# Kernel optimization log

Measured on AMD Instinct MI355X. Metric: run time of the kernel, lower is better.

## Reference

```python
import math
from collections import deque
import jax, jax.numpy as jnp
import numpy as np

PS = 16; DF = 256; DS = 16; DLANG = 896; BETA = 2.0
B_SZ = 2; IMG = 512


def setup_inputs():
    key = jax.random.key(0)
    ks = jax.random.split(key, 16)
    def rn(k, shape, scale=1.0):
        return jax.random.normal(k, shape, jnp.float32) * scale
    # W_delta bias init: inverse-softplus of dt ~ LogUniform(1e-3, 1e-1), as in torch _init_weights
    u = jax.random.uniform(ks[15], (DF,), jnp.float32)
    dt = jnp.exp(u * (math.log(0.1) - math.log(0.001)) + math.log(0.001))
    inv_dt = dt + jnp.log(-jnp.expm1(-dt))
    return {
        "images": rn(ks[0], (B_SZ, 3, IMG, IMG)),
        "lang_g": rn(ks[1], (B_SZ, DLANG)),
        "conv1_w": rn(ks[2], (64, 3, 3, 3), 1.0 / math.sqrt(27)),
        "conv1_b": jnp.zeros((64,), jnp.float32),
        "conv2_w": rn(ks[3], (128, 64, 3, 3), 1.0 / math.sqrt(576)),
        "conv2_b": jnp.zeros((128,), jnp.float32),
        "fc_w": rn(ks[4], (DF, 128), 1.0 / math.sqrt(128)),
        "fc_b": jnp.zeros((DF,), jnp.float32),
        "W_gate": rn(ks[5], (DF, DLANG), 1.0 / math.sqrt(DLANG)),
        "W_g_prime": rn(ks[6], (DF, DLANG), 1.0 / math.sqrt(DLANG)),
        "A_log": jnp.log(jnp.broadcast_to(jnp.arange(1, DS + 1, dtype=jnp.float32), (DF, DS))),
        "D": jnp.ones((DF,), jnp.float32),
        "B_w": rn(ks[7], (DS, DF), 1.0 / math.sqrt(DF)),
        "B_b": jnp.zeros((DS,), jnp.float32),
        "C_w": rn(ks[8], (DS, DF), 1.0 / math.sqrt(DF)),
        "C_b": jnp.zeros((DS,), jnp.float32),
        "Wd_w": rn(ks[9], (DF, DF), 1.0 / math.sqrt(DF)),
        "Wd_b": inv_dt,
        "out_w": rn(ks[10], (DF, DF), 1.0 / math.sqrt(DF)),
        "out_b": jnp.zeros((DF,), jnp.float32),
        "ln_g": jnp.ones((DF,), jnp.float32),
        "ln_b": jnp.zeros((DF,), jnp.float32),
    }


def _gelu(x):
    return jax.nn.gelu(x, approximate=False)  # torch nn.GELU() default = exact erf


def _conv(x, w, b):
    y = jax.lax.conv_general_dilated(x, w, (1, 1), 'SAME', dimension_numbers=('NCHW', 'OIHW', 'NCHW'))
    return y + b[None, :, None, None]


def _patch_feats(images, c1w, c1b, c2w, c2b, fcw, fcb):
    B, C, H, W = images.shape
    nH, nW = H // PS, W // PS
    # non-overlapping patchify (== unfold/unfold in torch)
    p = images.reshape(B, C, nH, PS, nW, PS).transpose(0, 2, 4, 1, 3, 5).reshape(B * nH * nW, C, PS, PS)
    h = _gelu(_conv(p, c1w, c1b))
    h = _gelu(_conv(h, c2w, c2b))
    h = h.mean(axis=(2, 3))  # AdaptiveAvgPool2d((1,1))
    feats = (h @ fcw.T + fcb).reshape(B, nH * nW, DF)
    return feats, nH, nW


def _structure(feats, r_sem, nH, nW):
    # Host-side (numpy) Kruskal MST + BFS ordering, mirroring the torch detach().cpu() path.
    f = np.asarray(feats, np.float32)
    r = np.asarray(r_sem, np.float32)
    B, P, _ = f.shape
    src, dst = [], []
    for i in range(nH):
        for j in range(nW):
            u = i * nW + j
            if j + 1 < nW:
                src.append(u); dst.append(u + 1)
            if i + 1 < nH:
                src.append(u); dst.append(u + nW)
    src = np.array(src); dst = np.array(dst)
    bfs_all, par_all = [], []
    for b in range(B):
        fn = f[b] / np.maximum(np.linalg.norm(f[b], axis=1, keepdims=True), 1e-12)
        cos = (fn[src] * fn[dst]).sum(1)
        w = (1.0 - r[b][src]) * (1.0 - r[b][dst]) * (-cos) + 1e-6
        parent = np.arange(P)
        def find(x):
            while parent[x] != x:
                parent[x] = parent[parent[x]]
                x = parent[x]
            return x
        adj = [[] for _ in range(P)]
        cnt = 0
        for idx in np.argsort(w):
            ru, rv = find(int(src[idx])), find(int(dst[idx]))
            if ru != rv:
                parent[ru] = rv
                adj[src[idx]].append(int(dst[idx]))
                adj[dst[idx]].append(int(src[idx]))
                cnt += 1
                if cnt == P - 1:
                    break
        root = int(r[b].argmax())
        vis = [False] * P; par_of = [-1] * P; bfs = []
        q = deque([root]); vis[root] = True
        while q:
            n = q.popleft()
            bfs.append(n)
            for nb in adj[n]:
                if not vis[nb]:
                    vis[nb] = True
                    par_of[nb] = n
                    q.append(nb)
        o2b = [0] * P
        for bi, oi in enumerate(bfs):
            o2b[oi] = bi
        par_bfs = [-1 if par_of[o] == -1 else o2b[par_of[o]] for o in bfs]
        bfs_all.append(bfs); par_all.append(par_bfs)
    return jnp.array(bfs_all, jnp.int32), jnp.array(par_all, jnp.int32)


def _core(feats, r_sem, g_prime, bfs, par, A_log, D, B_w, B_b, C_w, C_b, Wd_w, Wd_b, out_w, out_b, ln_g, ln_b):
    A = -jnp.exp(A_log)  # (DF, DS)
    def one(f_b, r_b, gp, bfs_b, par_b):
        rs = r_b[bfs_b]                                  # (P,)
        X = f_b[bfs_b] + rs[:, None] * gp[None, :]       # (P, DF)
        delta = jax.nn.softplus(X @ Wd_w.T + Wd_b) * (1.0 + BETA * rs[:, None])
        Bp = X @ B_w.T + B_b                             # (P, DS)
        Cp = X @ C_w.T + C_b                             # (P, DS)
        P = X.shape[0]
        def body(H, inp):
            i, d_i, b_i, c_i, x_i, p_i = inp
            A_bar = jnp.exp(d_i[:, None] * A)            # (DF, DS)
            h_par = H[jnp.maximum(p_i, 0)] * (p_i >= 0)  # zeros at root
            h = A_bar * h_par + (d_i[:, None] * b_i[None, :]) * x_i[:, None]
            H = H.at[i].set(h)
            y = (h * c_i[None, :]).sum(-1) + D * x_i
            return H, y
        H0 = jnp.zeros((P, DF, DS), X.dtype)
        _, Y = jax.lax.scan(body, H0, (jnp.arange(P), delta, Bp, Cp, X, par_b))
        Yr = jnp.zeros_like(Y).at[bfs_b].set(Y)          # scatter back to raster order
        o = Yr @ out_w.T + out_b
        mu = o.mean(-1, keepdims=True)
        v = ((o - mu) ** 2).mean(-1, keepdims=True)
        return ln_g * (o - mu) / jnp.sqrt(v + 1e-5) + ln_b
    return jax.vmap(one)(feats, r_sem, g_prime, bfs, par)


def reference(images, lang_g, conv1_w, conv1_b, conv2_w, conv2_b, fc_w, fc_b, W_gate, W_g_prime, A_log, D, B_w, B_b, C_w, C_b, Wd_w, Wd_b, out_w, out_b, ln_g, ln_b):
    feats, nH, nW = _patch_feats(images, conv1_w, conv1_b, conv2_w, conv2_b, fc_w, fc_b)
    g_proj = lang_g @ W_gate.T
    r_sem = jax.nn.sigmoid(jnp.einsum('bd,bpd->bp', g_proj, feats) / math.sqrt(DF))
    bfs, par = _structure(feats, r_sem, nH, nW)
    g_prime = lang_g @ W_g_prime.T
    return _core(feats, r_sem, g_prime, bfs, par, A_log, D, B_w, B_b, C_w, C_b, Wd_w, Wd_b, out_w, out_b, ln_g, ln_b)
```

## Files before the change

kernel.cpp:

```cpp
#include <hip/hip_runtime.h>
#include <cstddef>
#include <cstdint>

#define NB    2
#define NP    1024
#define DFEAT 256
#define DSTATE 16
#define NEDGE 1984

typedef unsigned short ushortb;

typedef float fx16 __attribute__((ext_vector_type(16)));
typedef short s16x8 __attribute__((ext_vector_type(8)));

__device__ __forceinline__ float bf2f(unsigned short u){
  union { unsigned int i; float f; } c; c.i = ((unsigned int)u) << 16; return c.f;
}
__device__ __forceinline__ unsigned short f2bf(float f){
  union { float f; unsigned int i; } c; c.f = f;
  unsigned int u = c.i;
  unsigned int r = (u + 0x7fffu + ((u >> 16) & 1u)) >> 16;
  return (unsigned short)r;
}
__device__ __forceinline__ float ldin(const void* p, size_t i, int isbf){
  return isbf ? bf2f(((const ushortb*)p)[i]) : ((const float*)p)[i];
}
__device__ __forceinline__ float gelu_f(float x){
  return 0.5f * x * (1.0f + erff(x * 0.70710678118654752f));
}
__device__ __forceinline__ unsigned int f2sort(float f){
  union { float f; unsigned int i; } c; c.f = f;
  return (c.i & 0x80000000u) ? ~c.i : (c.i | 0x80000000u);
}

constexpr size_t AL(size_t x){ return (x + 63) & ~(size_t)63; }
constexpr size_t O_W1    = 0;
constexpr size_t O_B1    = AL(O_W1 + 1728);
constexpr size_t O_W2    = AL(O_B1 + 64);
constexpr size_t O_B2    = AL(O_W2 + 73728);
constexpr size_t O_FCW   = AL(O_B2 + 128);
constexpr size_t O_FCB   = AL(O_FCW + 32768);
constexpr size_t O_WDW   = AL(O_FCB + 256);
constexpr size_t O_WDB   = AL(O_WDW + 65536);
constexpr size_t O_BWO   = AL(O_WDB + 256);
constexpr size_t O_BBO   = AL(O_BWO + 4096);
constexpr size_t O_CWO   = AL(O_BBO + 16);
constexpr size_t O_CBO   = AL(O_CWO + 4096);
constexpr size_t O_OW    = AL(O_CBO + 16);
constexpr size_t O_OB    = AL(O_OW + 65536);
constexpr size_t O_AF    = AL(O_OB + 256);
constexpr size_t O_DD    = AL(O_AF + 4096);
constexpr size_t O_LNG   = AL(O_DD + 256);
constexpr size_t O_LNB   = AL(O_LNG + 256);
constexpr size_t O_FEATS = AL(O_LNB + 256);
constexpr size_t O_GPROJ = AL(O_FEATS + (size_t)NB*NP*DFEAT);
constexpr size_t O_GPRIM = AL(O_GPROJ + NB*DFEAT);
constexpr size_t O_RSEM  = AL(O_GPRIM + NB*DFEAT);
constexpr size_t O_BFS   = AL(O_RSEM + NB*NP);
constexpr size_t O_PAR   = AL(O_BFS + NB*NP);
constexpr size_t O_X     = AL(O_PAR + NB*NP);
constexpr size_t O_DELTA = AL(O_X + (size_t)NB*NP*DFEAT);
constexpr size_t O_BP    = AL(O_DELTA + (size_t)NB*NP*DFEAT);
constexpr size_t O_CP    = AL(O_BP + NB*NP*DSTATE);
constexpr size_t O_YR    = AL(O_CP + NB*NP*DSTATE);
constexpr size_t O_FLAG  = AL(O_YR + (size_t)NB*NP*DFEAT);
constexpr size_t O_LVL   = AL(O_FLAG + 64);

__global__ __launch_bounds__(256) void k_sniff(const void* img, float* ws)
{
  __shared__ int cnt;
  int tid = threadIdx.x;
  if (tid == 0) cnt = 0;
  __syncthreads();
  const ushortb* u = (const ushortb*)img;
  int local = 0;
  for (int k = 0; k < 16; k++){
    unsigned short v = u[tid * 16 + k];
    if (v == 0 || v == 0x8000u){ local++; continue; }
    float f = fabsf(bf2f(v));
    if (f >= 1e-8f && f <= 64.f) local++;
  }
  atomicAdd(&cnt, local);
  __syncthreads();
  if (tid == 0) ((int*)(ws + O_FLAG))[0] = (cnt >= 3900) ? 1 : 0;
}

__global__ __launch_bounds__(256) void k_convert(const void* c1w, const void* c1b, const void* c2w,
                          const void* c2b, const void* fcw, const void* fcb,
                          const void* alog, const void* dvec,
                          const void* bw, const void* bb, const void* cw, const void* cb,
                          const void* wdw, const void* wdb,
                          const void* ow, const void* ob,
                          const void* lng, const void* lnb,
                          const void* lang, const void* wgate, const void* wgp,
                          float* ws)
{
  const int F = ((const int*)(ws + O_FLAG))[0];
  if (blockIdx.x >= 3038){
    int row = (blockIdx.x - 3038) * 4 + (threadIdx.x >> 6);
    int lane = threadIdx.x & 63;
    int mat = row >> 9;
    int b   = (row >> 8) & 1;
    int df  = row & 255;
    const void* W = mat ? wgp : wgate;
    float s = 0.f;
    for (int k = lane; k < 896; k += 64)
      s += ldin(lang, (size_t)b * 896 + k, F) * ldin(W, (size_t)df * 896 + k, F);
    s += __shfl_xor(s, 1);  s += __shfl_xor(s, 2);  s += __shfl_xor(s, 4);
    s += __shfl_xor(s, 8);  s += __shfl_xor(s, 16); s += __shfl_xor(s, 32);
    if (lane == 0) ws[(mat ? O_GPRIM : O_GPROJ) + b * 256 + df] = s;
    return;
  }
  if (blockIdx.x >= 990){
    size_t i2 = (size_t)(blockIdx.x - 990) * 256 + threadIdx.x;
    if (i2 < (size_t)NB * NP * DFEAT) ws[O_YR + i2] = 0.f;
    return;
  }
  int i = blockIdx.x * 256 + threadIdx.x;
  if (i < 1728){ ws[O_W1 + i] = ldin(c1w, i, F); return; } i -= 1728;
  if (i < 64){ ws[O_B1 + i] = ldin(c1b, i, F); return; } i -= 64;
  if (i < 73728){
    int sg = i >> 11;
    int r = i & 2047;
    int nt = r >> 9;
    int r2 = r & 511;
    int ln = r2 >> 3, e = r2 & 7;
    int c  = sg / 18, s = sg - c * 18;
    int tap = s >> 1, ksub = s & 1;
    int oc = nt * 32 + (ln & 31);
    int ic = c * 32 + ksub * 16 + (ln >> 5) * 8 + e;
    float v = ldin(c2w, (size_t)(oc * 64 + ic) * 9 + tap, F);
    ushortb hi = f2bf(v);
    float lo = v - bf2f(hi);
    ushortb* WB = (ushortb*)(ws + O_W2);
    size_t cb = ((size_t)(sg * 4 + nt)) * 2;
    WB[cb * 512 + r2]       = hi;
    WB[(cb + 1) * 512 + r2] = f2bf(lo);
    return;
  } i -= 73728;
  if (i < 128){ ws[O_B2 + i] = ldin(c2b, i, F); return; } i -= 128;
  if (i < 32768){ ws[O_FCW + i] = ldin(fcw, i, F); return; } i -= 32768;
  if (i < 256){ ws[O_FCB + i] = ldin(fcb, i, F); return; } i -= 256;
  if (i < 65536){
    int k = i >> 8, df = i & 255;
    ws[O_WDW + i] = ldin(wdw, (size_t)df * 256 + k, F); return;
  } i -= 65536;
  if (i < 256){ ws[O_WDB + i] = ldin(wdb, i, F); return; } i -= 256;
  if (i < 4096){
    int k = i >> 4, s = i & 15;
    ws[O_BWO + i] = ldin(bw, (size_t)s * 256 + k, F); return;
  } i -= 4096;
  if (i < 16){ ws[O_BBO + i] = ldin(bb, i, F); return; } i -= 16;
  if (i < 4096){
    int k = i >> 4, s = i & 15;
    ws[O_CWO + i] = ldin(cw, (size_t)s * 256 + k, F); return;
  } i -= 4096;
  if (i < 16){ ws[O_CBO + i] = ldin(cb, i, F); return; } i -= 16;
  if (i < 65536){
    int k = i >> 8, df = i & 255;
    ws[O_OW + i] = ldin(ow, (size_t)df * 256 + k, F); return;
  } i -= 65536;
  if (i < 256){ ws[O_OB + i] = ldin(ob, i, F); return; } i -= 256;
  if (i < 4096){ ws[O_AF + i] = -expf(ldin(alog, i, F)); return; } i -= 4096;
  if (i < 256){ ws[O_DD + i] = ldin(dvec, i, F); return; } i -= 256;
  if (i < 256){ ws[O_LNG + i] = ldin(lng, i, F); return; } i -= 256;
  if (i < 256){ ws[O_LNB + i] = ldin(lnb, i, F); }
}

__global__ __launch_bounds__(512, 4) void k_patch(const void* __restrict__ img,
                                                  const float* __restrict__ ws,
                                                  float* __restrict__ feats)
{
  __shared__ __align__(16) ushortb Abuf[2 * 10368];
  __shared__ float timg[768];
  __shared__ float pool8[8 * 128];
  __shared__ float pm[128];
  const int F = ((const int*)(ws + O_FLAG))[0];
  const float* W1 = ws + O_W1;  const float* B1 = ws + O_B1;
  const float* FCW = ws + O_FCW; const float* FCB = ws + O_FCB;
  const s16x8* BF = (const s16x8*)(ws + O_W2);

  int blk = blockIdx.x; int b = blk >> 10; int pidx = blk & 1023;
  int ph = pidx >> 5, pw = pidx & 31;
  int tid = threadIdx.x;

  if (tid < 256){
    int y = tid >> 4, x = tid & 15;
    #pragma unroll
    for (int c = 0; c < 3; c++)
      timg[c * 256 + tid] =
        ldin(img, (((size_t)b * 3 + c) * 512 + (ph * 16 + y)) * 512 + (pw * 16 + x), F);
  }
  {
    uint4 z4 = make_uint4(0u, 0u, 0u, 0u);
    for (int r = tid; r < 324; r += 512){
      int y = r / 18, x = r - y * 18;
      if (y == 0 || y == 17 || x == 0 || x == 17){
        #pragma unroll
        for (int m = 0; m < 4; m++){
          *(uint4*)&Abuf[r * 32 + m * 8] = z4;
          *(uint4*)&Abuf[10368 + r * 32 + m * 8] = z4;
        }
      }
    }
  }
  __syncthreads();

  int wv = tid >> 6, ln = tid & 63;
  int l31 = ln & 31, lhi = ln >> 5;
  int xcol = ln & 15, yrow = l31 >> 4;
  int p = tid & 255, og = tid >> 8;
  int ii = p >> 4, jj = p & 15;

  float pin[27];
  #pragma unroll
  for (int cc = 0; cc < 3; cc++)
    #pragma unroll
    for (int dy = 0; dy < 3; dy++)
      #pragma unroll
      for (int dx = 0; dx < 3; dx++){
        int y = ii + dy - 1, x = jj + dx - 1;
        bool ok = (y >= 0 && y < 16 && x >= 0 && x < 16);
        pin[cc * 9 + dy * 3 + dx] = ok ? timg[cc * 256 + y * 16 + x] : 0.f;
      }
  int rw = (ii + 1) * 18 + (jj + 1);
  int swz = ((rw >> 1) & 3) << 3;

  #pragma unroll
  for (int pass = 0; pass < 2; pass++){
    fx16 acc0, acc1;
    #pragma unroll
    for (int r = 0; r < 16; r++){ acc0[r] = 0.f; acc1[r] = 0.f; }

    for (int c = 0; c < 2; c++){
      {
        int oc0 = c * 32 + og * 16;
        int w1base = __builtin_amdgcn_readfirstlane(oc0 * 27);
        const float* W1g = W1 + w1base;
        #pragma unroll
        for (int g = 0; g < 2; g++){
          float av[8];
          #pragma unroll
          for (int o = 0; o < 8; o++){
            float a = B1[oc0 + g * 8 + o];
            #pragma unroll
            for (int t = 0; t < 27; t++) a += W1g[(g * 8 + o) * 27 + t] * pin[t];
            av[o] = gelu_f(a);
          }
          unsigned int hp[4], lp[4];
          #pragma unroll
          for (int q = 0; q < 4; q++){
            float v0 = av[2 * q], v1 = av[2 * q + 1];
            ushortb h0 = f2bf(v0), h1 = f2bf(v1);
            float l0 = v0 - bf2f(h0), l1 = v1 - bf2f(h1);
            hp[q] = (unsigned int)h0 | ((unsigned int)h1 << 16);
            lp[q] = (unsigned int)f2bf(l0) | ((unsigned int)f2bf(l1) << 16);
          }
          int idx = rw * 32 + (((og * 2 + g) << 3) ^ swz);
          *(uint4*)&Abuf[idx] = make_uint4(hp[0], hp[1], hp[2], hp[3]);
          *(uint4*)&Abuf[10368 + idx] = make_uint4(lp[0], lp[1], lp[2], lp[3]);
        }
      }
      __syncthreads();

      {
        const s16x8* bfp = BF + (size_t)((c * 144 + pass * 4) * 64 + ln);
        for (int s = 0; s < 18; s++){
          int tap = s >> 1, ksub = s & 1;
          int dyq = tap / 3, dxq = tap - dyq * 3;
          int icq0 = (ksub << 1) + lhi;
          int rA = (wv * 2 + yrow + dyq) * 18 + (xcol + dxq);
          int iA = rA * 32 + ((icq0 ^ ((rA >> 1) & 3)) << 3);
          s16x8 fa_h = *(const s16x8*)&Abuf[iA];
          s16x8 fa_l = *(const s16x8*)&Abuf[10368 + iA];
          const s16x8* bq = bfp + (s << 9);
          s16x8 fb0h = bq[0];
          s16x8 fb0l = bq[64];
          s16x8 fb1h = bq[128];
          s16x8 fb1l = bq[192];
          acc0 = __builtin_amdgcn_mfma_f32_32x32x16_bf16(fa_h, fb0h, acc0, 0, 0, 0);
          acc1 = __builtin_amdgcn_mfma_f32_32x32x16_bf16(fa_h, fb1h, acc1, 0, 0, 0);
          acc0 = __builtin_amdgcn_mfma_f32_32x32x16_bf16(fa_l, fb0h, acc0, 0, 0, 0);
          acc1 = __builtin_amdgcn_mfma_f32_32x32x16_bf16(fa_l, fb1h, acc1, 0, 0, 0);
          acc0 = __builtin_amdgcn_mfma_f32_32x32x16_bf16(fa_h, fb0l, acc0, 0, 0, 0);
          acc1 = __builtin_amdgcn_mfma_f32_32x32x16_bf16(fa_h, fb1l, acc1, 0, 0, 0);
        }
      }
      __syncthreads();
    }

    #pragma unroll
    for (int n = 0; n < 2; n++){
      int nt = pass * 2 + n;
      float bz = ws[O_B2 + nt * 32 + l31];
      float sum = 0.f;
      #pragma unroll
      for (int r = 0; r < 16; r++)
        sum += gelu_f(((n == 0) ? acc0[r] : acc1[r]) + bz);
      sum += __shfl_xor(sum, 32);
      if (lhi == 0) pool8[wv * 128 + nt * 32 + l31] = sum;
    }
  }
  __syncthreads();
  if (tid < 128){
    float sv = 0.f;
    #pragma unroll
    for (int w = 0; w < 8; w++) sv += pool8[w * 128 + tid];
    pm[tid] = sv * (1.f / 256.f);
  }
  __syncthreads();

  if (tid < 256){
    int df = tid;
    float s = FCB[df];
    const float* wrow = FCW + (size_t)df * 128;
    #pragma unroll
    for (int k = 0; k < 128; k += 4)
      s += wrow[k] * pm[k] + wrow[k + 1] * pm[k + 1]
         + wrow[k + 2] * pm[k + 2] + wrow[k + 3] * pm[k + 3];
    feats[((size_t)(b * 1024 + pidx)) * 256 + df] = s;
  }
}

__device__ __forceinline__ void edge_uv(int e, int& u, int& v){
  if (e < 1953){
    int i = e / 63; int k = e - i * 63;
    if (k < 62){ int j = k >> 1; u = i * 32 + j; v = (k & 1) ? u + 32 : u + 1; }
    else { u = i * 32 + 31; v = u + 32; }
  } else { u = 31 * 32 + (e - 1953); v = u + 1; }
}

__global__ __launch_bounds__(1024) void k_struct(float* __restrict__ ws)
{
  __shared__ float s_ninv[1024];
  __shared__ float s_w[NEDGE];
  __shared__ float s_r[1024];
  __shared__ int   s_comp[1024];
  __shared__ int   s_link[1024];
  __shared__ int   s_link2[1024];
  __shared__ unsigned long long s_best[1024];
  __shared__ unsigned char  s_mst[NEDGE];
  __shared__ unsigned short s_adj[1024 * 4];
  __shared__ unsigned char  s_deg[1024];
  __shared__ unsigned short s_bfs[1024];
  __shared__ short          s_parof[1024];
  __shared__ unsigned short s_o2b[1024];
  __shared__ unsigned short s_cur[1024];
  __shared__ unsigned short s_nxt[1024];
  __shared__ unsigned short s_off[1025];
  __shared__ unsigned short s_loff2[1026];
  __shared__ unsigned long long s_rootkey;
  __shared__ int s_ncomp, s_cursz, s_bfscnt, s_nextsz, s_nlvl;

  int b = blockIdx.x; int tid = threadIdx.x;
  const float* feats = ws + O_FEATS + (size_t)b * NP * DFEAT;

  {
    const float4* f4 = (const float4*)(feats + (size_t)tid * 256);
    const float4* g4 = (const float4*)(ws + O_GPROJ + b * 256);
    float d = 0.f, gdot = 0.f;
    for (int k = 0; k < 64; k++){
      float4 q = f4[k]; float4 g = g4[k];
      d += q.x*q.x + q.y*q.y + q.z*q.z + q.w*q.w;
      gdot += q.x*g.x + q.y*g.y + q.z*g.z + q.w*g.w;
    }
    s_ninv[tid] = 1.f / fmaxf(sqrtf(d), 1e-12f);
    float r = 1.f / (1.f + expf(-gdot * (1.f / 16.f)));
    s_r[tid] = r;
    ws[O_RSEM + b * NP + tid] = r;
    s_comp[tid] = tid;
    s_deg[tid] = 0;
    s_bfs[tid] = (unsigned short)tid;
    s_o2b[tid] = (unsigned short)tid;
    s_parof[tid] = -1;
  }
  for (int e = tid; e < NEDGE; e += 1024) s_mst[e] = 0;
  __syncthreads();

  for (int e = tid; e < NEDGE; e += 1024){
    int u, v; edge_uv(e, u, v);
    const float4* fu = (const float4*)(feats + (size_t)u * 256);
    const float4* fv = (const float4*)(feats + (size_t)v * 256);
    float d = 0.f;
    for (int k = 0; k < 64; k++){ float4 a = fu[k], c = fv[k]; d += a.x*c.x + a.y*c.y + a.z*c.z + a.w*c.w; }
    float cosv = d * s_ninv[u] * s_ninv[v];
    s_w[e] = (1.f - s_r[u]) * (1.f - s_r[v]) * (-cosv) + 1e-6f;
  }
  __syncthreads();

  for (int round = 0; round < 12; round++){
    s_best[tid] = ~0ull;
    __syncthreads();
    for (int e = tid; e < NEDGE; e += 1024){
      int u, v; edge_uv(e, u, v);
      int cu = s_comp[u], cv = s_comp[v];
      if (cu != cv){
        unsigned long long key = (((unsigned long long)f2sort(s_w[e])) << 32) | (unsigned int)e;
        atomicMin(&s_best[cu], key);
        atomicMin(&s_best[cv], key);
      }
    }
    __syncthreads();
    int l = tid;
    if (s_comp[tid] == tid && s_best[tid] != ~0ull){
      int e = (int)(s_best[tid] & 0xffffffffu);
      int u, v; edge_uv(e, u, v);
      s_mst[e] = 1;
      int cu = s_comp[u], cv = s_comp[v];
      l = (cu == tid) ? cv : cu;
    }
    s_link[tid] = l;
    __syncthreads();
    if (l != tid && s_link[l] == tid && tid < l) s_link[tid] = tid;
    __syncthreads();
    {
      int x = tid;
      int p = s_link[x];
      while (p != x){ x = p; p = s_link[x]; }
      s_link2[tid] = x;
    }
    __syncthreads();
    s_comp[tid] = s_link2[s_comp[tid]];
    if (tid == 0) s_ncomp = 0;
    __syncthreads();
    if (s_comp[tid] == tid) atomicAdd(&s_ncomp, 1);
    __syncthreads();
    if (s_ncomp == 1) break;
    __syncthreads();
  }
  __syncthreads();

  {
    int v = tid; int i = v >> 5, j = v & 31;
    float wloc[4]; int nloc[4]; int d = 0;
    if (j > 0){ int e = (i < 31) ? (i * 63 + 2 * (j - 1)) : (1953 + (j - 1));
      if (s_mst[e]){ wloc[d] = s_w[e]; nloc[d] = v - 1; d++; } }
    if (j < 31){ int e = (i < 31) ? (i * 63 + 2 * j) : (1953 + j);
      if (s_mst[e]){ wloc[d] = s_w[e]; nloc[d] = v + 1; d++; } }
    if (i > 0){ int e = (i - 1) * 63 + ((j < 31) ? (2 * j + 1) : 62);
      if (s_mst[e]){ wloc[d] = s_w[e]; nloc[d] = v - 32; d++; } }
    if (i < 31){ int e = i * 63 + ((j < 31) ? (2 * j + 1) : 62);
      if (s_mst[e]){ wloc[d] = s_w[e]; nloc[d] = v + 32; d++; } }
    for (int a = 1; a < d; a++){
      float wv = wloc[a]; int nv = nloc[a]; int c = a - 1;
      while (c >= 0 && wloc[c] > wv){ wloc[c+1] = wloc[c]; nloc[c+1] = nloc[c]; c--; }
      wloc[c+1] = wv; nloc[c+1] = nv;
    }
    s_deg[v] = (unsigned char)d;
    for (int a = 0; a < d; a++) s_adj[v * 4 + a] = (unsigned short)nloc[a];
  }
  if (tid == 0) s_rootkey = 0ull;
  __syncthreads();
  {
    unsigned long long key = (((unsigned long long)f2sort(s_r[tid])) << 32) | (unsigned int)(1023 - tid);
    atomicMax(&s_rootkey, key);
  }
  __syncthreads();
  int root = 1023 - (int)(s_rootkey & 0xffffffffu);

  if (tid == 0){
    s_bfs[0] = (unsigned short)root; s_o2b[root] = 0; s_parof[root] = -1;
    s_cur[0] = (unsigned short)root; s_cursz = 1; s_bfscnt = 1; s_nlvl = 0;
  }
  __syncthreads();
  for (int lev = 0; lev < 1024; lev++){
    int csz = s_cursz;
    if (csz <= 0) break;
    if (tid < 64){
      int runbase = 0;
      for (int t0 = 0; t0 < csz; t0 += 64){
        int t = t0 + tid;
        int cnt = 0;
        if (t < csz){
          int n = s_cur[t];
          cnt = (int)s_deg[n] - (s_parof[n] >= 0 ? 1 : 0);
        }
        int v = cnt;
        #pragma unroll
        for (int off = 1; off < 64; off <<= 1){
          int u2 = __shfl_up(v, off);
          if (tid >= off) v += u2;
        }
        if (t < csz) s_off[t] = (unsigned short)(runbase + v - cnt);
        runbase += __shfl(v, 63);
      }
      if (tid == 0){
        if (s_nlvl < 1025){ s_loff2[s_nlvl] = (unsigned short)(s_bfscnt - csz); }
        s_nlvl++;
        s_nextsz = runbase;
      }
    }
    __syncthreads();
    if (tid < csz){
      int n = s_cur[tid]; int base = s_off[tid]; int k = 0;
      int pn = s_parof[n]; int dg = s_deg[n];
      for (int a = 0; a < dg; a++){
        int c = s_adj[n * 4 + a];
        if (c == pn) continue;
        s_parof[c] = (short)n;
        if (base + k < 1024) s_nxt[base + k] = (unsigned short)c;
        int pos = s_bfscnt + base + k;
        if (pos < 1024){
          s_bfs[pos] = (unsigned short)c;
          s_o2b[c] = (unsigned short)pos;
        }
        k++;
      }
    }
    __syncthreads();
    if (tid == 0){ s_bfscnt += s_nextsz; s_cursz = (s_nextsz > 1024) ? 1024 : s_nextsz; }
    __syncthreads();
    if (tid < s_cursz) s_cur[tid] = s_nxt[tid];
    __syncthreads();
  }
  __syncthreads();

  int* BFSo = (int*)(ws + O_BFS);
  int* PARo = (int*)(ws + O_PAR);
  {
    int node = s_bfs[tid] & 1023;
    BFSo[b * 1024 + tid] = node;
    int p = s_parof[node];
    PARo[b * 1024 + tid] = (p < 0) ? -1 : (int)(s_o2b[p] & 1023);
  }
  {
    int* LVLo = (int*)(ws + O_LVL) + b * 1040;
    int nl = s_nlvl; if (nl > 1024) nl = 1024;
    if (tid == 0){ LVLo[0] = nl; LVLo[1 + nl] = NP; }
    if (tid < nl) LVLo[1 + tid] = (int)s_loff2[tid];
  }
}

__global__ __launch_bounds__(256) void k_xdelta(float* __restrict__ ws)
{
  __shared__ float xs[256];
  int blk = blockIdx.x; int b = blk >> 10, i = blk & 1023; int df = threadIdx.x;
  const int* BFSo = (const int*)(ws + O_BFS);
  int node = BFSo[b * 1024 + i] & 1023;
  float rs = ws[O_RSEM + b * 1024 + node];
  float xv = ws[O_FEATS + ((size_t)(b * 1024 + node)) * 256 + df] + rs * ws[O_GPRIM + b * 256 + df];
  xs[df] = xv;
  ws[O_X + ((size_t)(b * 1024 + i)) * 256 + df] = xv;
  __syncthreads();
  {
    const float* WT = ws + O_WDW;
    float z = ws[O_WDB + df];
    #pragma unroll 8
    for (int k = 0; k < 256; k++)
      z += WT[(size_t)k * 256 + df] * xs[k];
    float sp = fmaxf(z, 0.f) + log1pf(expf(-fabsf(z)));
    ws[O_DELTA + ((size_t)(b * 1024 + i)) * 256 + df] = sp * (1.f + 2.f * rs);
  }
  if (df < 32){
    int s = df & 15;
    const float* WT = ws + ((df < 16) ? O_BWO : O_CWO);
    float a = ws[((df < 16) ? O_BBO : O_CBO) + s];
    #pragma unroll 8
    for (int k = 0; k < 256; k++) a += WT[k * 16 + s] * xs[k];
    ws[((df < 16) ? O_BP : O_CP) + (size_t)(b * 1024 + i) * 16 + s] = a;
  }
}

__global__ __launch_bounds__(256) void k_scan(float* __restrict__ ws)
{
  __shared__ float h[NP * DSTATE];
  __shared__ float xs[NP];
  __shared__ float ds[NP];
  __shared__ int   par_s[NP];
  __shared__ int   bfs_s[NP];
  int blk = blockIdx.x; int b = blk >> 8, f = blk & 255;
  int tid = threadIdx.x;
  int g = tid >> 4, s = tid & 15;
  const int* PARo = (const int*)(ws + O_PAR);
  const int* BFSo = (const int*)(ws + O_BFS);
  const int* LVLo = (const int*)(ws + O_LVL) + b * 1040;
  for (int i = tid; i < NP; i += 256){
    xs[i] = ws[O_X     + ((size_t)(b * NP + i)) * DFEAT + f];
    ds[i] = ws[O_DELTA + ((size_t)(b * NP + i)) * DFEAT + f];
    par_s[i] = PARo[b * NP + i];
    bfs_s[i] = BFSo[b * NP + i] & 1023;
  }
  __syncthreads();

  int nlvl = LVLo[0];
  bool degen = (nlvl < 1 || nlvl > NP);
  if (degen) nlvl = NP;

  float Aln = ws[O_AF + f * 16 + s];
  float Dv  = ws[O_DD + f];
  const float* Bp = ws + O_BP + (size_t)b * NP * DSTATE;
  const float* Cp = ws + O_CP + (size_t)b * NP * DSTATE;
  float* Yr = ws + O_YR + (size_t)b * NP * DFEAT;

  for (int l = 0; l < nlvl; l++){
    int o0, o1;
    if (degen){ o0 = l; o1 = l + 1; }
    else {
      o0 = LVLo[1 + l]; o1 = LVLo[2 + l];
      o0 = (o0 < 0) ? 0 : ((o0 > NP) ? NP : o0);
      o1 = (o1 < o0) ? o0 : ((o1 > NP) ? NP : o1);
    }
    for (int i = o0 + g; i < o1; i += 16){
      int p = par_s[i];
      float d = ds[i], x = xs[i];
      float hp = (p >= 0 && p < i) ? h[p * 16 + s] : 0.f;
      float hn = expf(d * Aln) * hp + d * Bp[i * 16 + s] * x;
      h[i * 16 + s] = hn;
      float t = hn * Cp[i * 16 + s];
      t += __shfl_xor(t, 1); t += __shfl_xor(t, 2);
      t += __shfl_xor(t, 4); t += __shfl_xor(t, 8);
      if (s == 0) Yr[(size_t)bfs_s[i] * DFEAT + f] = t + Dv * x;
    }
    __syncthreads();
  }
}

__global__ __launch_bounds__(256) void k_outln(const float* __restrict__ ws,
                                               void* __restrict__ out)
{
  __shared__ float yl[256];
  __shared__ float red[8];
  const int F = ((const int*)(ws + O_FLAG))[0];
  int blk = blockIdx.x; int b = blk >> 10, p = blk & 1023; int df = threadIdx.x;
  yl[df] = ws[O_YR + ((size_t)(b * 1024 + p)) * 256 + df];
  __syncthreads();
  const float* OT = ws + O_OW;
  float a = ws[O_OB + df];
  #pragma unroll 8
  for (int k = 0; k < 256; k++)
    a += OT[(size_t)k * 256 + df] * yl[k];
  int lane = df & 63, wid = df >> 6;
  float t = a;
  t += __shfl_xor(t, 1); t += __shfl_xor(t, 2);  t += __shfl_xor(t, 4);
  t += __shfl_xor(t, 8); t += __shfl_xor(t, 16); t += __shfl_xor(t, 32);
  if (lane == 0) red[wid] = t;
  __syncthreads();
  float mu = (red[0] + red[1] + red[2] + red[3]) * (1.f / 256.f);
  float dv = a - mu;
  float t2 = dv * dv;
  t2 += __shfl_xor(t2, 1); t2 += __shfl_xor(t2, 2);  t2 += __shfl_xor(t2, 4);
  t2 += __shfl_xor(t2, 8); t2 += __shfl_xor(t2, 16); t2 += __shfl_xor(t2, 32);
  if (lane == 0) red[4 + wid] = t2;
  __syncthreads();
  float var = (red[4] + red[5] + red[6] + red[7]) * (1.f / 256.f);
  float o = ws[O_LNG + df] * dv / sqrtf(var + 1e-5f) + ws[O_LNB + df];
  size_t idx = ((size_t)(b * 1024 + p)) * 256 + df;
  if (F) ((ushortb*)out)[idx] = f2bf(o);
  else   ((float*)out)[idx]   = o;
}

extern "C" void kernel_launch(void* const* d_in, const int* in_sizes, int n_in,
                              void* d_out, int out_size, void* d_ws, size_t ws_size,
                              hipStream_t stream)
{
  (void)in_sizes; (void)n_in; (void)out_size; (void)ws_size;
  const void* img   = d_in[0];
  const void* lang  = d_in[1];
  const void* c1w   = d_in[2];
  const void* c1b   = d_in[3];
  const void* c2w   = d_in[4];
  const void* c2b   = d_in[5];
  const void* fcw   = d_in[6];
  const void* fcb   = d_in[7];
  const void* wgate = d_in[8];
  const void* wgp   = d_in[9];
  const void* alog  = d_in[10];
  const void* dvec  = d_in[11];
  const void* bw    = d_in[12];
  const void* bb    = d_in[13];
  const void* cw    = d_in[14];
  const void* cb    = d_in[15];
  const void* wdw   = d_in[16];
  const void* wdb   = d_in[17];
  const void* ow    = d_in[18];
  const void* ob    = d_in[19];
  const void* lng   = d_in[20];
  const void* lnb   = d_in[21];
  float* ws = (float*)d_ws;

  k_sniff<<<1, 256, 0, stream>>>(img, ws);
  k_convert<<<990 + 2048 + 256, 256, 0, stream>>>(c1w, c1b, c2w, c2b, fcw, fcb, alog, dvec,
                                                  bw, bb, cw, cb, wdw, wdb, ow, ob, lng, lnb,
                                                  lang, wgate, wgp, ws);
  k_patch<<<2048, 512, 0, stream>>>(img, ws, ws + O_FEATS);
  k_struct<<<2, 1024, 0, stream>>>(ws);
  k_xdelta<<<2048, 256, 0, stream>>>(ws);
  k_scan<<<NB * DFEAT, 256, 0, stream>>>(ws);
  k_outln<<<2048, 256, 0, stream>>>(ws, d_out);
}
```

Before: 850.8 us.

## Overlap per-node projections with graph structure kernel and restructure patch conv tiling

```diff
diff --git a/kernel.cpp b/kernel.cpp
--- a/kernel.cpp
+++ b/kernel.cpp
@@ -171,9 +171,9 @@
                                                   const float* __restrict__ ws,
                                                   float* __restrict__ feats)
 {
-  __shared__ __align__(16) ushortb Abuf[2 * 10368];
+  __shared__ __align__(16) ushortb Abuf[2 * 11520];
   __shared__ float timg[768];
-  __shared__ float pool8[8 * 128];
+  __shared__ float pool8[512];
   __shared__ float pm[128];
   const int F = ((const int*)(ws + O_FLAG))[0];
   const float* W1 = ws + O_W1;  const float* B1 = ws + O_B1;
@@ -183,6 +183,7 @@
   int blk = blockIdx.x; int b = blk >> 10; int pidx = blk & 1023;
   int ph = pidx >> 5, pw = pidx & 31;
   int tid = threadIdx.x;
+  uint4 z4 = make_uint4(0u, 0u, 0u, 0u);
 
   if (tid < 256){
     int y = tid >> 4, x = tid & 15;
@@ -191,122 +192,126 @@
       timg[c * 256 + tid] =
         ldin(img, (((size_t)b * 3 + c) * 512 + (ph * 16 + y)) * 512 + (pw * 16 + x), F);
   }
-  {
-    uint4 z4 = make_uint4(0u, 0u, 0u, 0u);
-    for (int r = tid; r < 324; r += 512){
-      int y = r / 18, x = r - y * 18;
-      if (y == 0 || y == 17 || x == 0 || x == 17){
-        #pragma unroll
-        for (int m = 0; m < 4; m++){
-          *(uint4*)&Abuf[r * 32 + m * 8] = z4;
-          *(uint4*)&Abuf[10368 + r * 32 + m * 8] = z4;
-        }
-      }
-    }
+  for (int z = tid; z < 320; z += 512){
+    int plane = z / 160; int z2 = z - plane * 160;
+    int cell = z2 >> 3, q = z2 & 7;
+    int lr = cell >> 1; int gc = (cell & 1) ? 17 : 0;
+    *(uint4*)&Abuf[plane * 11520 + ((lr * 18 + gc) << 6) + (q << 3)] = z4;
   }
   __syncthreads();
 
   int wv = tid >> 6, ln = tid & 63;
   int l31 = ln & 31, lhi = ln >> 5;
   int xcol = ln & 15, yrow = l31 >> 4;
-  int p = tid & 255, og = tid >> 8;
-  int ii = p >> 4, jj = p & 15;
-
-  float pin[27];
-  #pragma unroll
-  for (int cc = 0; cc < 3; cc++)
-    #pragma unroll
-    for (int dy = 0; dy < 3; dy++)
+  int mt = wv >> 1, ng = wv & 1;
+
+  float psum0 = 0.f, psum1 = 0.f;
+
+  for (int h = 0; h < 2; h++){
+    {
+      int pr = h ? 9 : 0;
+      for (int z = tid; z < 256; z += 512){
+        int plane = z >> 7; int z2 = z & 127;
+        int gc = 1 + (z2 >> 3); int q = z2 & 7;
+        *(uint4*)&Abuf[plane * 11520 + ((pr * 18 + gc) << 6) + (q << 3)] = z4;
+      }
+    }
+    for (int u = tid; u < 1152; u += 512){
+      int og = u / 144; int px = u - og * 144;
+      int r9 = px >> 4, col = px & 15;
+      int ir = h ? (7 + r9) : r9;
+      float pin[27];
       #pragma unroll
-      for (int dx = 0; dx < 3; dx++){
-        int y = ii + dy - 1, x = jj + dx - 1;
-        bool ok = (y >= 0 && y < 16 && x >= 0 && x < 16);
-        pin[cc * 9 + dy * 3 + dx] = ok ? timg[cc * 256 + y * 16 + x] : 0.f;
+      for (int cc = 0; cc < 3; cc++)
+        #pragma unroll
+        for (int dy = 0; dy < 3; dy++)
+          #pragma unroll
+          for (int dx = 0; dx < 3; dx++){
+            int y = ir + dy - 1, x = col + dx - 1;
+            bool ok = (y >= 0 && y < 16 && x >= 0 && x < 16);
+            pin[cc * 9 + dy * 3 + dx] = ok ? timg[cc * 256 + y * 16 + x] : 0.f;
+          }
+      int oc0 = og * 8;
+      float av[8];
+      #pragma unroll
+      for (int o = 0; o < 8; o++){
+        float a = B1[oc0 + o];
+        #pragma unroll
+        for (int t = 0; t < 27; t++) a += W1[(oc0 + o) * 27 + t] * pin[t];
+        av[o] = gelu_f(a);
       }
-  int rw = (ii + 1) * 18 + (jj + 1);
-  int swz = ((rw >> 1) & 3) << 3;
-
-  #pragma unroll
-  for (int pass = 0; pass < 2; pass++){
+      unsigned int hp[4], lp[4];
+      #pragma unroll
+      for (int q = 0; q < 4; q++){
+        float v0 = av[2 * q], v1 = av[2 * q + 1];
+        ushortb h0 = f2bf(v0), h1 = f2bf(v1);
+        float l0 = v0 - bf2f(h0), l1 = v1 - bf2f(h1);
+        hp[q] = (unsigned int)h0 | ((unsigned int)h1 << 16);
+        lp[q] = (unsigned int)f2bf(l0) | ((unsigned int)f2bf(l1) << 16);
+      }
+      int lr = h ? r9 : (r9 + 1);
+      int gc = col + 1;
+      int idx = ((lr * 18 + gc) << 6) + ((og ^ (gc & 7)) << 3);
+      *(uint4*)&Abuf[idx] = make_uint4(hp[0], hp[1], hp[2], hp[3]);
+      *(uint4*)&Abuf[11520 + idx] = make_uint4(lp[0], lp[1], lp[2], lp[3]);
+    }
+    __syncthreads();
+
     fx16 acc0, acc1;
     #pragma unroll
     for (int r = 0; r < 16; r++){ acc0[r] = 0.f; acc1[r] = 0.f; }
-
-    for (int c = 0; c < 2; c++){
-      {
-        int oc0 = c * 32 + og * 16;
-        int w1base = __builtin_amdgcn_readfirstlane(oc0 * 27);
-        const float* W1g = W1 + w1base;
-        #pragma unroll
-        for (int g = 0; g < 2; g++){
-          float av[8];
-          #pragma unroll
-          for (int o = 0; o < 8; o++){
-            float a = B1[oc0 + g * 8 + o];
-            #pragma unroll
-            for (int t = 0; t < 27; t++) a += W1g[(g * 8 + o) * 27 + t] * pin[t];
-            av[o] = gelu_f(a);
-          }
-          unsigned int hp[4], lp[4];
-          #pragma unroll
-          for (int q = 0; q < 4; q++){
-            float v0 = av[2 * q], v1 = av[2 * q + 1];
-            ushortb h0 = f2bf(v0), h1 = f2bf(v1);
-            float l0 = v0 - bf2f(h0), l1 = v1 - bf2f(h1);
-            hp[q] = (unsigned int)h0 | ((unsigned int)h1 << 16);
-            lp[q] = (unsigned int)f2bf(l0) | ((unsigned int)f2bf(l1) << 16);
-          }
-          int idx = rw * 32 + (((og * 2 + g) << 3) ^ swz);
-          *(uint4*)&Abuf[idx] = make_uint4(hp[0], hp[1], hp[2], hp[3]);
-          *(uint4*)&Abuf[10368 + idx] = make_uint4(lp[0], lp[1], lp[2], lp[3]);
-        }
+    for (int s = 0; s < 36; s++){
+      int tap = s >> 2, icsub = s & 3;
+      int dyq = tap / 3, dxq = tap - dyq * 3;
+      int lr = 2 * mt + yrow + dyq;
+      int gc = xcol + dxq;
+      int slot = (icsub << 1) + lhi;
+      int iA = ((lr * 18 + gc) << 6) + ((slot ^ (gc & 7)) << 3);
+      s16x8 fa_h = *(const s16x8*)&Abuf[iA];
+      s16x8 fa_l = *(const s16x8*)&Abuf[11520 + iA];
+      int sg = (icsub >> 1) * 18 + (tap << 1) + (icsub & 1);
+      const s16x8* bq = BF + (size_t)(((sg * 4 + ng * 2) * 2) * 64 + ln);
+      s16x8 fb0h = bq[0];
+      s16x8 fb0l = bq[64];
+      s16x8 fb1h = bq[128];
+      s16x8 fb1l = bq[192];
+      acc0 = __builtin_amdgcn_mfma_f32_32x32x16_bf16(fa_h, fb0h, acc0, 0, 0, 0);
+      acc1 = __builtin_amdgcn_mfma_f32_32x32x16_bf16(fa_h, fb1h, acc1, 0, 0, 0);
+      acc0 = __builtin_amdgcn_mfma_f32_32x32x16_bf16(fa_l, fb0h, acc0, 0, 0, 0);
+      acc1 = __builtin_amdgcn_mfma_f32_32x32x16_bf16(fa_l, fb1h, acc1, 0, 0, 0);
+      acc0 = __builtin_amdgcn_mfma_f32_32x32x16_bf16(fa_h, fb0l, acc0, 0, 0, 0);
+      acc1 = __builtin_amdgcn_mfma_f32_32x32x16_bf16(fa_h, fb1l, acc1, 0, 0, 0);
+    }
+    {
+      float bz0 = ws[O_B2 + (ng * 2) * 32 + l31];
+      float bz1 = ws[O_B2 + (ng * 2 + 1) * 32 + l31];
+      float s0 = 0.f, s1 = 0.f;
+      #pragma unroll
+      for (int r = 0; r < 16; r++){
+        s0 += gelu_f(acc0[r] + bz0);
+        s1 += gelu_f(acc1[r] + bz1);
       }
-      __syncthreads();
-
-      {
-        const s16x8* bfp = BF + (size_t)((c * 144 + pass * 4) * 64 + ln);
-        for (int s = 0; s < 18; s++){
-          int tap = s >> 1, ksub = s & 1;
-          int dyq = tap / 3, dxq = tap - dyq * 3;
-          int icq0 = (ksub << 1) + lhi;
-          int rA = (wv * 2 + yrow + dyq) * 18 + (xcol + dxq);
-          int iA = rA * 32 + ((icq0 ^ ((rA >> 1) & 3)) << 3);
-          s16x8 fa_h = *(const s16x8*)&Abuf[iA];
-          s16x8 fa_l = *(const s16x8*)&Abuf[10368 + iA];
-          const s16x8* bq = bfp + (s << 9);
-          s16x8 fb0h = bq[0];
-          s16x8 fb0l = bq[64];
-          s16x8 fb1h = bq[128];
-          s16x8 fb1l = bq[192];
-          acc0 = __builtin_amdgcn_mfma_f32_32x32x16_bf16(fa_h, fb0h, acc0, 0, 0, 0);
-          acc1 = __builtin_amdgcn_mfma_f32_32x32x16_bf16(fa_h, fb1h, acc1, 0, 0, 0);
-          acc0 = __builtin_amdgcn_mfma_f32_32x32x16_bf16(fa_l, fb0h, acc0, 0, 0, 0);
-          acc1 = __builtin_amdgcn_mfma_f32_32x32x16_bf16(fa_l, fb1h, acc1, 0, 0, 0);
-          acc0 = __builtin_amdgcn_mfma_f32_32x32x16_bf16(fa_h, fb0l, acc0, 0, 0, 0);
-          acc1 = __builtin_amdgcn_mfma_f32_32x32x16_bf16(fa_h, fb1l, acc1, 0, 0, 0);
-        }
-      }
-      __syncthreads();
-    }
-
-    #pragma unroll
-    for (int n = 0; n < 2; n++){
-      int nt = pass * 2 + n;
-      float bz = ws[O_B2 + nt * 32 + l31];
-      float sum = 0.f;
-      #pragma unroll
-      for (int r = 0; r < 16; r++)
-        sum += gelu_f(((n == 0) ? acc0[r] : acc1[r]) + bz);
-      sum += __shfl_xor(sum, 32);
-      if (lhi == 0) pool8[wv * 128 + nt * 32 + l31] = sum;
+      psum0 += s0; psum1 += s1;
+    }
+    __syncthreads();
+  }
+
+  {
+    float s0 = psum0 + __shfl_xor(psum0, 32);
+    float s1 = psum1 + __shfl_xor(psum1, 32);
+    if (lhi == 0){
+      pool8[wv * 64 + l31] = s0;
+      pool8[wv * 64 + 32 + l31] = s1;
     }
   }
   __syncthreads();
   if (tid < 128){
-    float sv = 0.f;
-    #pragma unroll
-    for (int w = 0; w < 8; w++) sv += pool8[w * 128 + tid];
-    pm[tid] = sv * (1.f / 256.f);
+    int oc = tid; int nt = oc >> 5; int ngo = nt >> 1; int n = nt & 1; int l = oc & 31;
+    float sv = pool8[(0 * 2 + ngo) * 64 + n * 32 + l]
+             + pool8[(1 * 2 + ngo) * 64 + n * 32 + l]
+             + pool8[(2 * 2 + ngo) * 64 + n * 32 + l]
+             + pool8[(3 * 2 + ngo) * 64 + n * 32 + l];
+    pm[oc] = sv * (1.f / 256.f);
   }
   __syncthreads();
 
@@ -330,7 +335,7 @@
   } else { u = 31 * 32 + (e - 1953); v = u + 1; }
 }
 
-__global__ __launch_bounds__(1024) void k_struct(float* __restrict__ ws)
+__global__ __launch_bounds__(1024) void k_sx(float* __restrict__ ws)
 {
   __shared__ float s_ninv[1024];
   __shared__ float s_w[NEDGE];
@@ -352,7 +357,48 @@
   __shared__ unsigned long long s_rootkey;
   __shared__ int s_ncomp, s_cursz, s_bfscnt, s_nextsz, s_nlvl;
 
-  int b = blockIdx.x; int tid = threadIdx.x;
+  int tid = threadIdx.x;
+
+  if (blockIdx.x >= 2){
+    int gi = (int)(blockIdx.x - 2) * 4 + (tid >> 8);
+    int b2 = gi >> 10, node = gi & 1023;
+    int df = tid & 255;
+    int wg = tid >> 8;
+    float f = ws[O_FEATS + ((size_t)(b2 * 1024 + node)) * 256 + df];
+    float v = f * ws[O_GPROJ + b2 * 256 + df];
+    v += __shfl_xor(v, 1);  v += __shfl_xor(v, 2);  v += __shfl_xor(v, 4);
+    v += __shfl_xor(v, 8);  v += __shfl_xor(v, 16); v += __shfl_xor(v, 32);
+    if ((tid & 63) == 0) s_w[tid >> 6] = v;
+    __syncthreads();
+    float gdot = s_w[wg * 4] + s_w[wg * 4 + 1] + s_w[wg * 4 + 2] + s_w[wg * 4 + 3];
+    float rs = 1.f / (1.f + expf(-gdot * (1.f / 16.f)));
+    float xv = f + rs * ws[O_GPRIM + b2 * 256 + df];
+    s_ninv[tid] = xv;
+    ws[O_X + (size_t)gi * 256 + df] = xv;
+    __syncthreads();
+    {
+      const float* WT = ws + O_WDW;
+      const float* xg = s_ninv + wg * 256;
+      float z = ws[O_WDB + df];
+      #pragma unroll 8
+      for (int k = 0; k < 256; k++)
+        z += WT[(size_t)k * 256 + df] * xg[k];
+      float sp = fmaxf(z, 0.f) + log1pf(expf(-fabsf(z)));
+      ws[O_DELTA + (size_t)gi * 256 + df] = sp * (1.f + 2.f * rs);
+    }
+    if (df < 32){
+      int s2 = df & 15;
+      const float* WT = ws + ((df < 16) ? O_BWO : O_CWO);
+      const float* xg = s_ninv + wg * 256;
+      float a = ws[((df < 16) ? O_BBO : O_CBO) + s2];
+      #pragma unroll 8
+      for (int k = 0; k < 256; k++) a += WT[k * 16 + s2] * xg[k];
+      ws[((df < 16) ? O_BP : O_CP) + (size_t)gi * 16 + s2] = a;
+    }
+    return;
+  }
+
+  int b = blockIdx.x;
   const float* feats = ws + O_FEATS + (size_t)b * NP * DFEAT;
 
   {
@@ -531,36 +577,6 @@
   }
 }
 
-__global__ __launch_bounds__(256) void k_xdelta(float* __restrict__ ws)
-{
-  __shared__ float xs[256];
-  int blk = blockIdx.x; int b = blk >> 10, i = blk & 1023; int df = threadIdx.x;
-  const int* BFSo = (const int*)(ws + O_BFS);
-  int node = BFSo[b * 1024 + i] & 1023;
-  float rs = ws[O_RSEM + b * 1024 + node];
-  float xv = ws[O_FEATS + ((size_t)(b * 1024 + node)) * 256 + df] + rs * ws[O_GPRIM + b * 256 + df];
-  xs[df] = xv;
-  ws[O_X + ((size_t)(b * 1024 + i)) * 256 + df] = xv;
-  __syncthreads();
-  {
-    const float* WT = ws + O_WDW;
-    float z = ws[O_WDB + df];
-    #pragma unroll 8
-    for (int k = 0; k < 256; k++)
-      z += WT[(size_t)k * 256 + df] * xs[k];
-    float sp = fmaxf(z, 0.f) + log1pf(expf(-fabsf(z)));
-    ws[O_DELTA + ((size_t)(b * 1024 + i)) * 256 + df] = sp * (1.f + 2.f * rs);
-  }
-  if (df < 32){
-    int s = df & 15;
-    const float* WT = ws + ((df < 16) ? O_BWO : O_CWO);
-    float a = ws[((df < 16) ? O_BBO : O_CBO) + s];
-    #pragma unroll 8
-    for (int k = 0; k < 256; k++) a += WT[k * 16 + s] * xs[k];
-    ws[((df < 16) ? O_BP : O_CP) + (size_t)(b * 1024 + i) * 16 + s] = a;
-  }
-}
-
 __global__ __launch_bounds__(256) void k_scan(float* __restrict__ ws)
 {
   __shared__ float h[NP * DSTATE];
@@ -575,10 +591,11 @@
   const int* BFSo = (const int*)(ws + O_BFS);
   const int* LVLo = (const int*)(ws + O_LVL) + b * 1040;
   for (int i = tid; i < NP; i += 256){
-    xs[i] = ws[O_X     + ((size_t)(b * NP + i)) * DFEAT + f];
-    ds[i] = ws[O_DELTA + ((size_t)(b * NP + i)) * DFEAT + f];
+    int node = BFSo[b * NP + i] & 1023;
+    bfs_s[i] = node;
     par_s[i] = PARo[b * NP + i];
-    bfs_s[i] = BFSo[b * NP + i] & 1023;
+    xs[i] = ws[O_X     + ((size_t)(b * NP + node)) * DFEAT + f];
+    ds[i] = ws[O_DELTA + ((size_t)(b * NP + node)) * DFEAT + f];
   }
   __syncthreads();
 
@@ -602,14 +619,15 @@
     }
     for (int i = o0 + g; i < o1; i += 16){
       int p = par_s[i];
+      int node = bfs_s[i];
       float d = ds[i], x = xs[i];
       float hp = (p >= 0 && p < i) ? h[p * 16 + s] : 0.f;
-      float hn = expf(d * Aln) * hp + d * Bp[i * 16 + s] * x;
+      float hn = expf(d * Aln) * hp + d * Bp[node * 16 + s] * x;
       h[i * 16 + s] = hn;
-      float t = hn * Cp[i * 16 + s];
+      float t = hn * Cp[node * 16 + s];
       t += __shfl_xor(t, 1); t += __shfl_xor(t, 2);
       t += __shfl_xor(t, 4); t += __shfl_xor(t, 8);
-      if (s == 0) Yr[(size_t)bfs_s[i] * DFEAT + f] = t + Dv * x;
+      if (s == 0) Yr[(size_t)node * DFEAT + f] = t + Dv * x;
     }
     __syncthreads();
   }
@@ -683,8 +701,7 @@
                                                   bw, bb, cw, cb, wdw, wdb, ow, ob, lng, lnb,
                                                   lang, wgate, wgp, ws);
   k_patch<<<2048, 512, 0, stream>>>(img, ws, ws + O_FEATS);
-  k_struct<<<2, 1024, 0, stream>>>(ws);
-  k_xdelta<<<2048, 256, 0, stream>>>(ws);
+  k_sx<<<2 + 512, 1024, 0, stream>>>(ws);
   k_scan<<<NB * DFEAT, 256, 0, stream>>>(ws);
   k_outln<<<2048, 256, 0, stream>>>(ws, d_out);
 }
```

Result: no change. 855.8 us (+0.6%).
